# Kernel optimization log

Measured on AMD Instinct MI355X. Metric: run time of the kernel, lower is better.

The kernel has to match this reference:

```python
import jax, jax.numpy as jnp
import numpy as np

H = 16  # heads
DH = 64  # dim_head
SCALE = DH ** -0.5


def rotate_half(x):
    x1, x2 = jnp.split(x, 2, axis=-1)
    return jnp.concatenate([-x2, x1], axis=-1)


def apply_rope(pos, t):
    # pos: [n, d] broadcast over [b, h, n, d]
    return t * jnp.cos(pos) + rotate_half(t) * jnp.sin(pos)


def setup_inputs() -> dict:
    key = jax.random.key(0)
    ks = jax.random.split(key, 6)
    B, N, D = 4, 2048, 1024
    inner = H * DH
    x = jax.random.normal(ks[0], (B, N, D), dtype=jnp.float32)
    rotary_emb = jax.random.normal(ks[1], (N, DH), dtype=jnp.float32)
    Wq = jax.random.normal(ks[2], (D, inner), dtype=jnp.float32) / np.sqrt(D)
    Wkv = jax.random.normal(ks[3], (D, 2 * inner), dtype=jnp.float32) / np.sqrt(D)
    Wout = jax.random.normal(ks[4], (inner, D), dtype=jnp.float32) / np.sqrt(inner)
    bout = jnp.zeros((D,), dtype=jnp.float32)
    return {"x": x, "rotary_emb": rotary_emb, "Wq": Wq, "Wkv": Wkv, "Wout": Wout, "bout": bout}


def reference(x, rotary_emb, Wq, Wkv, Wout, bout):
    B, N, D = x.shape
    # QKV projections (self-attention: context = x)
    q = x @ Wq                       # [b, n, h*d]
    kv = x @ Wkv                     # [b, n, 2*h*d]
    k, v = jnp.split(kv, 2, axis=-1)

    def to_heads(t):
        return t.reshape(B, N, H, DH).transpose(0, 2, 1, 3)  # [b, h, n, d]

    q, k, v = to_heads(q), to_heads(k), to_heads(v)
    q = apply_rope(rotary_emb, q)
    k = apply_rope(rotary_emb, k)

    # scaled dot-product attention
    scores = jnp.einsum('bhid,bhjd->bhij', q, k) * SCALE
    attn = jax.nn.softmax(scores, axis=-1)
    out = jnp.einsum('bhij,bhjd->bhid', attn, v)  # [b, h, n, d]
    out = out.transpose(0, 2, 1, 3).reshape(B, N, H * DH)
    return out @ Wout + bout
```

## Files before the change

kernel.cpp:

```cpp
#include <hip/hip_runtime.h>

#define BB 4
#define NN 2048
#define DD 1024
#define HH 16
#define DHH 64
#define MM (BB*NN)
#define QS 3072

typedef unsigned short u16;
typedef __attribute__((ext_vector_type(8))) short short8;
typedef __attribute__((ext_vector_type(4))) float floatx4;

#if __has_builtin(__builtin_amdgcn_exp2f)
#define EXP2F __builtin_amdgcn_exp2f
#else
#define EXP2F exp2f
#endif

__device__ __forceinline__ u16 f2bf(float f) {
  union { float f; unsigned u; } v; v.f = f;
  unsigned u = v.u;
  return (u16)((u + 0x7fffu + ((u >> 16) & 1u)) >> 16);
}
__device__ __forceinline__ float bf2f(u16 h) {
  union { unsigned u; float f; } v; v.u = ((unsigned)h) << 16;
  return v.f;
}
__device__ __forceinline__ unsigned fbits(float f) {
  union { float f; unsigned u; } v; v.f = f; return v.u;
}
__device__ __forceinline__ unsigned pkbf(float lo, float hi) {
#if __has_builtin(__builtin_amdgcn_perm)
  return __builtin_amdgcn_perm(fbits(hi), fbits(lo), 0x07060302u);
#else
  return (fbits(lo) >> 16) | (fbits(hi) & 0xffff0000u);
#endif
}
__device__ __forceinline__ void gll16(const u16* g, u16* l) {
  __builtin_amdgcn_global_load_lds((const __attribute__((address_space(1))) unsigned int*)g,
                                   (__attribute__((address_space(3))) unsigned int*)l, 16, 0, 0);
}
__device__ __forceinline__ int toff(int row, int kc) {
  int pr = row >> 1;
  int c = (((row & 1) << 2) + kc) ^ (pr & 7);
  return pr * 64 + c * 8;
}

#define SOFTMAX_SCALE 0.18033688f
#define SOFTMAX_BIAS  -28.8539008f

__global__ __launch_bounds__(256) void cvt_kernel(const float* __restrict__ in,
                                                  u16* __restrict__ out, int n) {
  int i = (blockIdx.x * 256 + threadIdx.x) * 4;
  if (i >= n) return;
  float4 v = *(const float4*)(in + i);
  u16 o[4] = {f2bf(v.x), f2bf(v.y), f2bf(v.z), f2bf(v.w)};
  *(uint2*)(out + i) = *(uint2*)o;
}

__global__ __launch_bounds__(256) void tcvt3_kernel(const float* __restrict__ Wq,
                                                    const float* __restrict__ Wkv,
                                                    const float* __restrict__ Wout,
                                                    u16* __restrict__ WT,
                                                    u16* __restrict__ WoutT) {
  __shared__ float t[64][65];
  int bx = blockIdx.x;
  const float* src;
  u16* dst;
  int C, c0;
  if (bx < 16)      { src = Wq;   dst = WT;                       C = 1024; c0 = bx * 64; }
  else if (bx < 48) { src = Wkv;  dst = WT + (size_t)DD * DD;     C = 2048; c0 = (bx - 16) * 64; }
  else              { src = Wout; dst = WoutT;                    C = 1024; c0 = (bx - 48) * 64; }
  const int R = 1024;
  int r0 = blockIdx.y * 64;
  int tid = threadIdx.x;
#pragma unroll
  for (int i = 0; i < 16; ++i) {
    int lin = i * 256 + tid;
    int rr = lin >> 6, cc = lin & 63;
    t[rr][cc] = src[(size_t)(r0 + rr) * C + c0 + cc];
  }
  __syncthreads();
#pragma unroll
  for (int i = 0; i < 16; ++i) {
    int lin = i * 256 + tid;
    int rr = lin >> 6, cc = lin & 63;
    dst[(size_t)(c0 + rr) * R + r0 + cc] = f2bf(t[cc][rr]);
  }
}

__global__ __launch_bounds__(256) void rope_tab_kernel(const float* __restrict__ rot,
                                                       float2* __restrict__ tab) {
  int i = blockIdx.x * 256 + threadIdx.x;
  float p = rot[i];
  float s, c;
  __sincosf(p, &s, &c);
  tab[i] = make_float2(c, s);
}

__global__ __launch_bounds__(512, 2) void gemm_qk(const u16* __restrict__ A,
                                                  const u16* __restrict__ Bt,
                                                  u16* __restrict__ qd,
                                                  u16* __restrict__ kd,
                                                  const float2* __restrict__ tab) {
  const int K = DD;
  const int NT = K / 64;
  __shared__ __align__(16) u16 lds[65536];
  int tid = threadIdx.x;
  int wave = tid >> 6, lane = tid & 63;
  int q4 = lane >> 4, l16 = lane & 15;
  int wr = wave >> 2, wc = wave & 3;

  int flat = blockIdx.y * 8 + blockIdx.x;
  int wg = (flat & 7) * 32 + (flat >> 3);
  int bx = wg & 7, by = wg >> 3;
  int m0 = by * 256, n0 = bx * 256;

  const u16* Ag = A + (size_t)m0 * K;
  const u16* Bg = Bt + (size_t)n0 * K;

  int spr = tid >> 3, sct = tid & 7, su = sct ^ (spr & 7);
  int srow = spr * 2 + (su >> 2);
  int skc = (su & 3) * 8;
  size_t so = (size_t)srow * K + skc;

  int toffA[8], toffB[4];
#pragma unroll
  for (int mi = 0; mi < 8; ++mi) toffA[mi] = wr * 4096 + toff(mi * 16 + l16, q4);
#pragma unroll
  for (int ni = 0; ni < 4; ++ni)
    toffB[ni] = (wc >> 1) * 4096 + toff((wc & 1) * 64 + ni * 16 + l16, q4);

  floatx4 acc[8][4];
#pragma unroll
  for (int mi = 0; mi < 8; ++mi)
#pragma unroll
    for (int ni = 0; ni < 4; ++ni) acc[mi][ni] = (floatx4){0.f, 0.f, 0.f, 0.f};

  auto stageHalf = [&](int t, int mat, int kh) {
    const u16* src = (mat ? Bg : Ag) + so + t * 64 + kh * 32;
    u16* dst = lds + (t & 1) * 32768 + mat * 16384 + kh * 8192 + wave * 512;
    gll16(src, dst);
    gll16(src + (size_t)128 * K, dst + 4096);
  };

  stageHalf(0, 1, 0); stageHalf(0, 0, 0); stageHalf(0, 1, 1); stageHalf(0, 0, 1);
  stageHalf(1, 1, 0); stageHalf(1, 0, 0); stageHalf(1, 1, 1);
  __builtin_amdgcn_s_waitcnt(0x0F76);
  __builtin_amdgcn_s_barrier();

#pragma unroll
  for (int t = 0; t < NT; ++t) {
    const u16* Ab = lds + (t & 1) * 32768;
    const u16* Bb = Ab + 16384;
    short8 af[4], bfq[4];

#pragma unroll
    for (int ni = 0; ni < 4; ++ni) bfq[ni] = *(const short8*)(Bb + toffB[ni]);
#pragma unroll
    for (int f = 0; f < 4; ++f) af[f] = *(const short8*)(Ab + toffA[f]);
    if (t + 1 < NT) stageHalf(t + 1, 0, 1);
    __builtin_amdgcn_s_barrier();
    __builtin_amdgcn_s_waitcnt(0xC07F);
    __builtin_amdgcn_s_setprio(1);
#pragma unroll
    for (int f = 0; f < 4; ++f)
#pragma unroll
      for (int ni = 0; ni < 4; ++ni)
        acc[f][ni] = __builtin_amdgcn_mfma_f32_16x16x32_bf16(bfq[ni], af[f], acc[f][ni], 0, 0, 0);
    __builtin_amdgcn_s_setprio(0);
    __builtin_amdgcn_s_barrier();

#pragma unroll
    for (int f = 0; f < 4; ++f) af[f] = *(const short8*)(Ab + toffA[4 + f]);
    if (t + 2 < NT) stageHalf(t + 2, 1, 0);
    __builtin_amdgcn_s_barrier();
    __builtin_amdgcn_s_waitcnt(0xC07F);
    __builtin_amdgcn_s_setprio(1);
#pragma unroll
    for (int f = 0; f < 4; ++f)
#pragma unroll
      for (int ni = 0; ni < 4; ++ni)
        acc[4 + f][ni] = __builtin_amdgcn_mfma_f32_16x16x32_bf16(bfq[ni], af[f], acc[4 + f][ni], 0, 0, 0);
    __builtin_amdgcn_s_setprio(0);
    __builtin_amdgcn_s_barrier();

#pragma unroll
    for (int ni = 0; ni < 4; ++ni) bfq[ni] = *(const short8*)(Bb + 8192 + toffB[ni]);
#pragma unroll
    for (int f = 0; f < 4; ++f) af[f] = *(const short8*)(Ab + 8192 + toffA[f]);
    if (t + 2 < NT) stageHalf(t + 2, 0, 0);
    __builtin_amdgcn_s_barrier();
    __builtin_amdgcn_s_waitcnt(0xC07F);
    __builtin_amdgcn_s_setprio(1);
#pragma unroll
    for (int f = 0; f < 4; ++f)
#pragma unroll
      for (int ni = 0; ni < 4; ++ni)
        acc[f][ni] = __builtin_amdgcn_mfma_f32_16x16x32_bf16(bfq[ni], af[f], acc[f][ni], 0, 0, 0);
    __builtin_amdgcn_s_setprio(0);
    __builtin_amdgcn_s_barrier();

#pragma unroll
    for (int f = 0; f < 4; ++f) af[f] = *(const short8*)(Ab + 8192 + toffA[4 + f]);
    if (t + 2 < NT) stageHalf(t + 2, 1, 1);
    __builtin_amdgcn_s_barrier();
    __builtin_amdgcn_s_waitcnt(0xC07F);
    __builtin_amdgcn_s_setprio(1);
#pragma unroll
    for (int f = 0; f < 4; ++f)
#pragma unroll
      for (int ni = 0; ni < 4; ++ni)
        acc[4 + f][ni] = __builtin_amdgcn_mfma_f32_16x16x32_bf16(bfq[ni], af[f], acc[4 + f][ni], 0, 0, 0);
    __builtin_amdgcn_s_setprio(0);
    if (t == NT - 2) __builtin_amdgcn_s_waitcnt(0x0F70);
    else if (t < NT - 2) __builtin_amdgcn_s_waitcnt(0x0F76);
    __builtin_amdgcn_s_barrier();
  }

  int h = (n0 + wc * 64) >> 6;
  u16* dst = (h < 16) ? qd : kd;
  int hh = h & 15;
  float scl = (h < 16) ? SOFTMAX_SCALE : 1.0f;
  int b = m0 >> 11;
  int tokbase = (m0 & (NN - 1)) + wr * 128;
#pragma unroll
  for (int mi = 0; mi < 8; ++mi) {
    int tok = tokbase + mi * 16 + l16;
    u16* rowp = dst + ((size_t)(b * HH + hh) * NN + tok) * 64;
    const float2* tb = tab + tok * 64;
#pragma unroll
    for (int ni = 0; ni < 2; ++ni) {
      int d0 = ni * 16 + q4 * 4;
      u16 plo[4], phi[4];
#pragma unroll
      for (int r = 0; r < 4; ++r) {
        float2 cs0 = tb[d0 + r];
        float2 cs1 = tb[d0 + r + 32];
        float v0 = acc[mi][ni][r], v1 = acc[mi][ni + 2][r];
        plo[r] = f2bf((v0 * cs0.x - v1 * cs0.y) * scl);
        phi[r] = f2bf((v1 * cs1.x + v0 * cs1.y) * scl);
      }
      *(uint2*)(rowp + d0) = *(uint2*)plo;
      *(uint2*)(rowp + d0 + 32) = *(uint2*)phi;
    }
  }
}

__global__ __launch_bounds__(256) void gemm_v(const u16* __restrict__ A,
                                              const u16* __restrict__ Bt,
                                              u16* __restrict__ vt) {
  const int K = DD;
  __shared__ __align__(16) u16 lds[16384];
  int tid = threadIdx.x;
  int wave = tid >> 6, lane = tid & 63;
  int q4 = lane >> 4, l16 = lane & 15;

  int flat = blockIdx.y * 8 + blockIdx.x;
  int wg = (flat & 7) * 64 + (flat >> 3);
  int bx = wg & 7, by = wg >> 3;
  int m0 = by * 128, n0 = bx * 128;

  int wm = (wave >> 1) * 64, wn = (wave & 1) * 64;

  const u16* Ag = A + (size_t)m0 * K;
  const u16* Bg = Bt + (size_t)(2048 + n0) * K;
  int o1 = tid, o2 = tid + 256;
  int pr1 = o1 >> 3, c1 = (o1 & 7) ^ (pr1 & 7);
  int row1 = pr1 * 2 + (c1 >> 2), kc1 = (c1 & 3) * 8;
  int pr2 = o2 >> 3, c2 = (o2 & 7) ^ (pr2 & 7);
  int row2 = pr2 * 2 + (c2 >> 2), kc2 = (c2 & 3) * 8;
  int d1 = wave * 512, d2 = 2048 + wave * 512;

  int foA[4], foB[4];
#pragma unroll
  for (int i = 0; i < 4; ++i) {
    foA[i] = toff(wm + i * 16 + l16, q4);
    foB[i] = toff(wn + i * 16 + l16, q4);
  }

  floatx4 acc[4][4];
#pragma unroll
  for (int mi = 0; mi < 4; ++mi)
#pragma unroll
    for (int ni = 0; ni < 4; ++ni) acc[mi][ni] = (floatx4){0.f, 0.f, 0.f, 0.f};

  gll16(Ag + (size_t)row1 * K + kc1, lds + d1);
  gll16(Ag + (size_t)row2 * K + kc2, lds + d2);
  gll16(Bg + (size_t)row1 * K + kc1, lds + 8192 + d1);
  gll16(Bg + (size_t)row2 * K + kc2, lds + 8192 + d2);

  for (int k0 = 0, it = 0; k0 < K; k0 += 32, ++it) {
    int boff = (it & 1) * 4096;
    if (k0 + 32 < K) {
      int nboff = 4096 - boff;
      int kn = k0 + 32;
      gll16(Ag + (size_t)row1 * K + kn + kc1, lds + nboff + d1);
      gll16(Ag + (size_t)row2 * K + kn + kc2, lds + nboff + d2);
      gll16(Bg + (size_t)row1 * K + kn + kc1, lds + 8192 + nboff + d1);
      gll16(Bg + (size_t)row2 * K + kn + kc2, lds + 8192 + nboff + d2);
      __builtin_amdgcn_s_waitcnt(0x0F74);
    } else {
      __builtin_amdgcn_s_waitcnt(0x0F70);
    }
    __builtin_amdgcn_s_barrier();
    const u16* Ac = lds + boff;
    const u16* Bc = lds + 8192 + boff;
    short8 af[4], bfr[4];
#pragma unroll
    for (int i = 0; i < 4; ++i) {
      af[i]  = *(const short8*)(Ac + foA[i]);
      bfr[i] = *(const short8*)(Bc + foB[i]);
    }
#pragma unroll
    for (int mi = 0; mi < 4; ++mi)
#pragma unroll
      for (int ni = 0; ni < 4; ++ni)
        acc[mi][ni] = __builtin_amdgcn_mfma_f32_16x16x32_bf16(af[mi], bfr[ni], acc[mi][ni], 0, 0, 0);
    __builtin_amdgcn_s_barrier();
  }

  int h = (n0 + wn) >> 6;
#pragma unroll
  for (int mi = 0; mi < 4; ++mi) {
    int mbase = m0 + wm + mi * 16 + q4 * 4;
    int b = mbase >> 11;
    int nn = mbase & (NN - 1);
    u16* base = vt + (size_t)(b * HH + h) * (NN * 64) + (nn >> 6) * 4096 + (nn & 63);
#pragma unroll
    for (int ni = 0; ni < 4; ++ni) {
      int d = ni * 16 + l16;
      u16 p[4] = {f2bf(acc[mi][ni][0]), f2bf(acc[mi][ni][1]),
                  f2bf(acc[mi][ni][2]), f2bf(acc[mi][ni][3])};
      *(uint2*)(base + d * 64) = *(uint2*)p;
    }
  }
}

__global__ __launch_bounds__(256) void gemm_out(const u16* __restrict__ A,
                                                const u16* __restrict__ Bt,
                                                float* __restrict__ Cout,
                                                const float* __restrict__ bias,
                                                int M, int N, int K) {
  __shared__ __align__(16) u16 lds[16384];
  int tid = threadIdx.x;
  int wave = tid >> 6, lane = tid & 63;
  int q4 = lane >> 4, l16 = lane & 15;
  int m0 = blockIdx.y * 128, n0 = blockIdx.x * 128;
  int wm = (wave >> 1) * 64, wn = (wave & 1) * 64;

  const u16* Ag = A + (size_t)m0 * K;
  const u16* Bg = Bt + (size_t)n0 * K;
  int o1 = tid, o2 = tid + 256;
  int pr1 = o1 >> 3, c1 = (o1 & 7) ^ (pr1 & 7);
  int row1 = pr1 * 2 + (c1 >> 2), kc1 = (c1 & 3) * 8;
  int pr2 = o2 >> 3, c2 = (o2 & 7) ^ (pr2 & 7);
  int row2 = pr2 * 2 + (c2 >> 2), kc2 = (c2 & 3) * 8;
  int d1 = wave * 512, d2 = 2048 + wave * 512;

  int foA[4], foB[4];
#pragma unroll
  for (int i = 0; i < 4; ++i) {
    foA[i] = toff(wm + i * 16 + l16, q4);
    foB[i] = toff(wn + i * 16 + l16, q4);
  }

  floatx4 acc[4][4];
#pragma unroll
  for (int mi = 0; mi < 4; ++mi)
#pragma unroll
    for (int ni = 0; ni < 4; ++ni) acc[mi][ni] = (floatx4){0.f, 0.f, 0.f, 0.f};

  gll16(Ag + (size_t)row1 * K + kc1, lds + d1);
  gll16(Ag + (size_t)row2 * K + kc2, lds + d2);
  gll16(Bg + (size_t)row1 * K + kc1, lds + 8192 + d1);
  gll16(Bg + (size_t)row2 * K + kc2, lds + 8192 + d2);

  for (int k0 = 0, it = 0; k0 < K; k0 += 32, ++it) {
    int boff = (it & 1) * 4096;
    if (k0 + 32 < K) {
      int nboff = 4096 - boff;
      int kn = k0 + 32;
      gll16(Ag + (size_t)row1 * K + kn + kc1, lds + nboff + d1);
      gll16(Ag + (size_t)row2 * K + kn + kc2, lds + nboff + d2);
      gll16(Bg + (size_t)row1 * K + kn + kc1, lds + 8192 + nboff + d1);
      gll16(Bg + (size_t)row2 * K + kn + kc2, lds + 8192 + nboff + d2);
      __builtin_amdgcn_s_waitcnt(0x0F74);
    } else {
      __builtin_amdgcn_s_waitcnt(0x0F70);
    }
    __builtin_amdgcn_s_barrier();
    const u16* Ac = lds + boff;
    const u16* Bc = lds + 8192 + boff;
    short8 af[4], bfr[4];
#pragma unroll
    for (int i = 0; i < 4; ++i) {
      af[i]  = *(const short8*)(Ac + foA[i]);
      bfr[i] = *(const short8*)(Bc + foB[i]);
    }
#pragma unroll
    for (int mi = 0; mi < 4; ++mi)
#pragma unroll
      for (int ni = 0; ni < 4; ++ni)
        acc[mi][ni] = __builtin_amdgcn_mfma_f32_16x16x32_bf16(af[mi], bfr[ni], acc[mi][ni], 0, 0, 0);
    __builtin_amdgcn_s_barrier();
  }

#pragma unroll
  for (int ni = 0; ni < 4; ++ni) {
    int col = n0 + wn + ni * 16 + l16;
    float bval = bias[col];
#pragma unroll
    for (int mi = 0; mi < 4; ++mi) {
#pragma unroll
      for (int r = 0; r < 4; ++r) {
        int row = m0 + wm + mi * 16 + q4 * 4 + r;
        Cout[(size_t)row * N + col] = acc[mi][ni][r] + bval;
      }
    }
  }
}

__global__ __launch_bounds__(512, 2) void attn_kernel(const u16* __restrict__ qd,
                                                      const u16* __restrict__ kd,
                                                      const u16* __restrict__ vt,
                                                      u16* __restrict__ ao) {
  __shared__ __align__(16) u16 lds[32768];

  int tid = threadIdx.x, wave = tid >> 6, lane = tid & 63;
  int q4 = lane >> 4, l16 = lane & 15;

  int F = blockIdx.y * 4 + blockIdx.x;
  int xcd = F & 7, r = F >> 3;
  int bh = xcd * 8 + (r >> 2);
  int qt = r & 3;
  int b = bh >> 4, h = bh & 15;

  const u16* qbh = qd + (size_t)bh * NN * 64;
  const u16* kbh = kd + (size_t)bh * NN * 64;
  const u16* vbh = vt + (size_t)bh * NN * 64;

  int srow = wave * 8 + (lane >> 3);
  int g = ((lane & 7) ^ ((lane >> 3) & 7)) * 8;
  int prow = ((srow >> 2) & 3) * 8 + ((srow >> 4) & 1) * 4 + (srow & 3) + ((srow >> 5) & 1) * 32;

#pragma unroll
  for (int it = 0; it < 8; ++it)
    gll16(qbh + (size_t)(qt * 512 + it * 64 + srow) * 64 + g, lds + (it * 64 + wave * 8) * 64);
  __builtin_amdgcn_s_waitcnt(0x0F70);
  __builtin_amdgcn_s_barrier();

  short8 aq[4][2];
#pragma unroll
  for (int mi = 0; mi < 4; ++mi)
#pragma unroll
    for (int ks = 0; ks < 2; ++ks) {
      int row = wave * 64 + mi * 16 + l16;
      aq[mi][ks] = *(const short8*)(lds + row * 64 + (((ks * 4 + q4) ^ (row & 7)) * 8));
    }
  __builtin_amdgcn_s_waitcnt(0xC07F);
  __builtin_amdgcn_s_barrier();

  auto stageKV = [&](int t) {
    gll16(kbh + (size_t)(t * 64 + prow) * 64 + g, lds + (t & 3) * 4096 + wave * 512);
    gll16(vbh + (size_t)t * 4096 + srow * 64 + g, lds + 16384 + (t & 3) * 4096 + wave * 512);
  };
  stageKV(0); stageKV(1);

  union { unsigned u[4]; short8 s8; } ones;
#pragma unroll
  for (int i = 0; i < 4; ++i) ones.u[i] = 0x3F803F80u;

  floatx4 lacc[4];
  floatx4 o[4][4];
#pragma unroll
  for (int mi = 0; mi < 4; ++mi) {
    lacc[mi] = (floatx4){0.f, 0.f, 0.f, 0.f};
#pragma unroll
    for (int di = 0; di < 4; ++di) o[mi][di] = (floatx4){0.f, 0.f, 0.f, 0.f};
  }

  const int NT = NN / 64;

  for (int t = 0; t < NT; ++t) {
    if (t < NT - 1) __builtin_amdgcn_s_waitcnt(0x0F72);
    else            __builtin_amdgcn_s_waitcnt(0x0F70);
    __builtin_amdgcn_s_barrier();
    if (t + 2 < NT) stageKV(t + 2);

    const u16* Kc = lds + (t & 3) * 4096;
    const u16* Vc = lds + 16384 + (t & 3) * 4096;

    floatx4 s[4][4];
#pragma unroll
    for (int kg = 0; kg < 4; ++kg)
#pragma unroll
      for (int mi = 0; mi < 4; ++mi)
        s[kg][mi] = (floatx4){SOFTMAX_BIAS, SOFTMAX_BIAS, SOFTMAX_BIAS, SOFTMAX_BIAS};
#pragma unroll
    for (int ks = 0; ks < 2; ++ks) {
      short8 kf[4];
#pragma unroll
      for (int kg = 0; kg < 4; ++kg) {
        int row = kg * 16 + l16;
        kf[kg] = *(const short8*)(Kc + row * 64 + (((ks * 4 + q4) ^ (row & 7)) * 8));
      }
#pragma unroll
      for (int kg = 0; kg < 4; ++kg)
#pragma unroll
        for (int mi = 0; mi < 4; ++mi)
          s[kg][mi] = __builtin_amdgcn_mfma_f32_16x16x32_bf16(kf[kg], aq[mi][ks], s[kg][mi], 0, 0, 0);
    }

    unsigned pk[4][4][2];
#pragma unroll
    for (int kg = 0; kg < 4; ++kg)
#pragma unroll
      for (int mi = 0; mi < 4; ++mi) {
        float e0 = EXP2F(s[kg][mi][0]);
        float e1 = EXP2F(s[kg][mi][1]);
        float e2 = EXP2F(s[kg][mi][2]);
        float e3 = EXP2F(s[kg][mi][3]);
        pk[kg][mi][0] = pkbf(e0, e1);
        pk[kg][mi][1] = pkbf(e2, e3);
      }

#pragma unroll
    for (int ks = 0; ks < 2; ++ks) {
      short8 vf[4];
#pragma unroll
      for (int di = 0; di < 4; ++di) {
        int row = di * 16 + l16;
        vf[di] = *(const short8*)(Vc + row * 64 + (((ks * 4 + q4) ^ (row & 7)) * 8));
      }
#pragma unroll
      for (int mi = 0; mi < 4; ++mi) {
        union { unsigned u[4]; short8 s8; } bw;
        bw.u[0] = pk[2 * ks][mi][0];
        bw.u[1] = pk[2 * ks][mi][1];
        bw.u[2] = pk[2 * ks + 1][mi][0];
        bw.u[3] = pk[2 * ks + 1][mi][1];
        lacc[mi] = __builtin_amdgcn_mfma_f32_16x16x32_bf16(ones.s8, bw.s8, lacc[mi], 0, 0, 0);
#pragma unroll
        for (int di = 0; di < 4; ++di)
          o[mi][di] = __builtin_amdgcn_mfma_f32_16x16x32_bf16(vf[di], bw.s8, o[mi][di], 0, 0, 0);
      }
    }
  }

#pragma unroll
  for (int mi = 0; mi < 4; ++mi) {
    float rinv = 1.0f / lacc[mi][0];
    int qrow = qt * 512 + wave * 64 + mi * 16 + l16;
    size_t base = (size_t)(b * NN + qrow) * DD + h * DHH + q4 * 4;
#pragma unroll
    for (int di = 0; di < 4; ++di) {
      u16 p[4] = {f2bf(o[mi][di][0] * rinv), f2bf(o[mi][di][1] * rinv),
                  f2bf(o[mi][di][2] * rinv), f2bf(o[mi][di][3] * rinv)};
      *(uint2*)(ao + base + di * 16) = *(uint2*)p;
    }
  }
}

extern "C" void kernel_launch(void* const* d_in, const int* in_sizes, int n_in,
                              void* d_out, int out_size, void* d_ws, size_t ws_size,
                              hipStream_t stream) {
  const float* x    = (const float*)d_in[0];
  const float* rot  = (const float*)d_in[1];
  const float* Wq   = (const float*)d_in[2];
  const float* Wkv  = (const float*)d_in[3];
  const float* Wout = (const float*)d_in[4];
  const float* bout = (const float*)d_in[5];
  float* out = (float*)d_out;

  char* ws = (char*)d_ws;
  size_t off = 0;
  auto alloc = [&](size_t bytes) {
    void* p = ws + off;
    off = (off + bytes + 255) & ~(size_t)255;
    return p;
  };
  u16*    xb    = (u16*)alloc((size_t)MM * DD * 2);
  u16*    WT    = (u16*)alloc((size_t)QS * DD * 2);
  u16*    WoutT = (u16*)alloc((size_t)DD * DD * 2);
  float2* tab   = (float2*)alloc((size_t)NN * DHH * 8);
  u16*    qdb   = (u16*)alloc((size_t)MM * DD * 2);
  u16*    kdb   = (u16*)alloc((size_t)MM * DD * 2);
  u16*    vtt   = (u16*)alloc((size_t)MM * DD * 2);
  u16*    ao    = (u16*)alloc((size_t)MM * DD * 2);

  cvt_kernel<<<(MM * DD / 4) / 256, 256, 0, stream>>>(x, xb, MM * DD);
  tcvt3_kernel<<<dim3(64, 16), 256, 0, stream>>>(Wq, Wkv, Wout, WT, WoutT);
  rope_tab_kernel<<<(NN * DHH) / 256, 256, 0, stream>>>(rot, tab);

  gemm_qk<<<dim3(8, 32), 512, 0, stream>>>(xb, WT, qdb, kdb, tab);
  gemm_v<<<dim3(8, 64), 256, 0, stream>>>(xb, WT, vtt);

  attn_kernel<<<dim3(NN / 512, BB * HH), 512, 0, stream>>>(qdb, kdb, vtt, ao);

  gemm_out<<<dim3(DD / 128, MM / 128), 256, 0, stream>>>(ao, WoutT, out, bout, MM, DD, DD);
}
```

Measured before the change: 259.9 us.

## Restructure output GEMM into 256x128 tiles with 8 waves and deeper pipelining

Rewrites the output projection GEMM to use 512-thread blocks computing 256x128 tiles with a K step of 64. It adds a two-stage LDS buffer, interleaves loads of sub-slices with MFMA phases, raises wave priority with setprio, and remaps block IDs across XCDs. Separately, the attention kernel now feeds the softmax bias constant directly as the first MFMA accumulator instead of pre-initialising the score registers. The GEMM change aims to improve data reuse and hide memory latency, at the cost of more LDS (96KB) and more complex barrier and waitcnt logic that must stay correct.

Result: no change. 260.7 us (+0.3%).

```diff
diff --git a/kernel.cpp b/kernel.cpp
--- a/kernel.cpp
+++ b/kernel.cpp
@@ -338,84 +338,138 @@
   }
 }
 
-__global__ __launch_bounds__(256) void gemm_out(const u16* __restrict__ A,
-                                                const u16* __restrict__ Bt,
-                                                float* __restrict__ Cout,
-                                                const float* __restrict__ bias,
-                                                int M, int N, int K) {
-  __shared__ __align__(16) u16 lds[16384];
+__global__ __launch_bounds__(512, 2) void gemm_out(const u16* __restrict__ A,
+                                                   const u16* __restrict__ Bt,
+                                                   float* __restrict__ Cout,
+                                                   const float* __restrict__ bias,
+                                                   int M, int N, int K) {
+  const int NT = DD / 64;
+  __shared__ __align__(16) u16 lds[49152];
   int tid = threadIdx.x;
   int wave = tid >> 6, lane = tid & 63;
   int q4 = lane >> 4, l16 = lane & 15;
-  int m0 = blockIdx.y * 128, n0 = blockIdx.x * 128;
-  int wm = (wave >> 1) * 64, wn = (wave & 1) * 64;
+  int wr = wave >> 2, wc = wave & 3;
+
+  int flat = blockIdx.y * 8 + blockIdx.x;
+  int wg = (flat & 7) * 32 + (flat >> 3);
+  int bx = wg & 7, by = wg >> 3;
+  int m0 = by * 256, n0 = bx * 128;
 
   const u16* Ag = A + (size_t)m0 * K;
   const u16* Bg = Bt + (size_t)n0 * K;
-  int o1 = tid, o2 = tid + 256;
-  int pr1 = o1 >> 3, c1 = (o1 & 7) ^ (pr1 & 7);
-  int row1 = pr1 * 2 + (c1 >> 2), kc1 = (c1 & 3) * 8;
-  int pr2 = o2 >> 3, c2 = (o2 & 7) ^ (pr2 & 7);
-  int row2 = pr2 * 2 + (c2 >> 2), kc2 = (c2 & 3) * 8;
-  int d1 = wave * 512, d2 = 2048 + wave * 512;
-
-  int foA[4], foB[4];
-#pragma unroll
-  for (int i = 0; i < 4; ++i) {
-    foA[i] = toff(wm + i * 16 + l16, q4);
-    foB[i] = toff(wn + i * 16 + l16, q4);
-  }
-
-  floatx4 acc[4][4];
-#pragma unroll
-  for (int mi = 0; mi < 4; ++mi)
-#pragma unroll
-    for (int ni = 0; ni < 4; ++ni) acc[mi][ni] = (floatx4){0.f, 0.f, 0.f, 0.f};
-
-  gll16(Ag + (size_t)row1 * K + kc1, lds + d1);
-  gll16(Ag + (size_t)row2 * K + kc2, lds + d2);
-  gll16(Bg + (size_t)row1 * K + kc1, lds + 8192 + d1);
-  gll16(Bg + (size_t)row2 * K + kc2, lds + 8192 + d2);
-
-  for (int k0 = 0, it = 0; k0 < K; k0 += 32, ++it) {
-    int boff = (it & 1) * 4096;
-    if (k0 + 32 < K) {
-      int nboff = 4096 - boff;
-      int kn = k0 + 32;
-      gll16(Ag + (size_t)row1 * K + kn + kc1, lds + nboff + d1);
-      gll16(Ag + (size_t)row2 * K + kn + kc2, lds + nboff + d2);
-      gll16(Bg + (size_t)row1 * K + kn + kc1, lds + 8192 + nboff + d1);
-      gll16(Bg + (size_t)row2 * K + kn + kc2, lds + 8192 + nboff + d2);
-      __builtin_amdgcn_s_waitcnt(0x0F74);
-    } else {
-      __builtin_amdgcn_s_waitcnt(0x0F70);
-    }
-    __builtin_amdgcn_s_barrier();
-    const u16* Ac = lds + boff;
-    const u16* Bc = lds + 8192 + boff;
-    short8 af[4], bfr[4];
-#pragma unroll
-    for (int i = 0; i < 4; ++i) {
-      af[i]  = *(const short8*)(Ac + foA[i]);
-      bfr[i] = *(const short8*)(Bc + foB[i]);
-    }
-#pragma unroll
-    for (int mi = 0; mi < 4; ++mi)
-#pragma unroll
-      for (int ni = 0; ni < 4; ++ni)
-        acc[mi][ni] = __builtin_amdgcn_mfma_f32_16x16x32_bf16(af[mi], bfr[ni], acc[mi][ni], 0, 0, 0);
-    __builtin_amdgcn_s_barrier();
-  }
-
-#pragma unroll
-  for (int ni = 0; ni < 4; ++ni) {
-    int col = n0 + wn + ni * 16 + l16;
+
+  int spr = tid >> 3, sct = tid & 7, su = sct ^ (spr & 7);
+  int srow = spr * 2 + (su >> 2);
+  int skc = (su & 3) * 8;
+  size_t so = (size_t)srow * K + skc;
+
+  int toffA[8], toffB[2];
+#pragma unroll
+  for (int mi = 0; mi < 8; ++mi) toffA[mi] = wr * 4096 + toff(mi * 16 + l16, q4);
+#pragma unroll
+  for (int ni = 0; ni < 2; ++ni) toffB[ni] = toff(wc * 32 + ni * 16 + l16, q4);
+
+  floatx4 acc[8][2];
+#pragma unroll
+  for (int mi = 0; mi < 8; ++mi)
+#pragma unroll
+    for (int ni = 0; ni < 2; ++ni) acc[mi][ni] = (floatx4){0.f, 0.f, 0.f, 0.f};
+
+  auto stageA = [&](int t, int kh) {
+    const u16* src = Ag + so + t * 64 + kh * 32;
+    u16* dst = lds + (t & 1) * 24576 + kh * 8192 + wave * 512;
+    gll16(src, dst);
+    gll16(src + (size_t)128 * K, dst + 4096);
+  };
+  auto stageB = [&](int t, int kh) {
+    const u16* src = Bg + so + t * 64 + kh * 32;
+    u16* dst = lds + (t & 1) * 24576 + 16384 + kh * 4096 + wave * 512;
+    gll16(src, dst);
+  };
+
+  stageA(0, 0); stageA(0, 1); stageB(0, 0); stageB(0, 1);
+  stageA(1, 0); stageB(1, 0); stageB(1, 1);
+  __builtin_amdgcn_s_waitcnt(0x0F74);
+  __builtin_amdgcn_s_barrier();
+
+#pragma unroll
+  for (int t = 0; t < NT; ++t) {
+    const u16* Ab = lds + (t & 1) * 24576;
+    const u16* Bb = Ab + 16384;
+    short8 af[4], bfq[2];
+
+#pragma unroll
+    for (int ni = 0; ni < 2; ++ni) bfq[ni] = *(const short8*)(Bb + toffB[ni]);
+#pragma unroll
+    for (int f = 0; f < 4; ++f) af[f] = *(const short8*)(Ab + toffA[f]);
+    if (t + 1 < NT) stageA(t + 1, 1);
+    __builtin_amdgcn_s_barrier();
+    __builtin_amdgcn_s_waitcnt(0xC07F);
+    __builtin_amdgcn_s_setprio(1);
+#pragma unroll
+    for (int f = 0; f < 4; ++f)
+#pragma unroll
+      for (int ni = 0; ni < 2; ++ni)
+        acc[f][ni] = __builtin_amdgcn_mfma_f32_16x16x32_bf16(af[f], bfq[ni], acc[f][ni], 0, 0, 0);
+    __builtin_amdgcn_s_setprio(0);
+    __builtin_amdgcn_s_barrier();
+
+#pragma unroll
+    for (int f = 0; f < 4; ++f) af[f] = *(const short8*)(Ab + toffA[4 + f]);
+    if (t + 2 < NT) stageB(t + 2, 0);
+    __builtin_amdgcn_s_barrier();
+    __builtin_amdgcn_s_waitcnt(0xC07F);
+    __builtin_amdgcn_s_setprio(1);
+#pragma unroll
+    for (int f = 0; f < 4; ++f)
+#pragma unroll
+      for (int ni = 0; ni < 2; ++ni)
+        acc[4 + f][ni] = __builtin_amdgcn_mfma_f32_16x16x32_bf16(af[f], bfq[ni], acc[4 + f][ni], 0, 0, 0);
+    __builtin_amdgcn_s_setprio(0);
+    __builtin_amdgcn_s_barrier();
+
+#pragma unroll
+    for (int ni = 0; ni < 2; ++ni) bfq[ni] = *(const short8*)(Bb + 4096 + toffB[ni]);
+#pragma unroll
+    for (int f = 0; f < 4; ++f) af[f] = *(const short8*)(Ab + 8192 + toffA[f]);
+    if (t + 2 < NT) stageA(t + 2, 0);
+    __builtin_amdgcn_s_barrier();
+    __builtin_amdgcn_s_waitcnt(0xC07F);
+    __builtin_amdgcn_s_setprio(1);
+#pragma unroll
+    for (int f = 0; f < 4; ++f)
+#pragma unroll
+      for (int ni = 0; ni < 2; ++ni)
+        acc[f][ni] = __builtin_amdgcn_mfma_f32_16x16x32_bf16(af[f], bfq[ni], acc[f][ni], 0, 0, 0);
+    __builtin_amdgcn_s_setprio(0);
+    __builtin_amdgcn_s_barrier();
+
+#pragma unroll
+    for (int f = 0; f < 4; ++f) af[f] = *(const short8*)(Ab + 8192 + toffA[4 + f]);
+    if (t + 2 < NT) stageB(t + 2, 1);
+    __builtin_amdgcn_s_barrier();
+    __builtin_amdgcn_s_waitcnt(0xC07F);
+    __builtin_amdgcn_s_setprio(1);
+#pragma unroll
+    for (int f = 0; f < 4; ++f)
+#pragma unroll
+      for (int ni = 0; ni < 2; ++ni)
+        acc[4 + f][ni] = __builtin_amdgcn_mfma_f32_16x16x32_bf16(af[f], bfq[ni], acc[4 + f][ni], 0, 0, 0);
+    __builtin_amdgcn_s_setprio(0);
+    if (t == NT - 2) __builtin_amdgcn_s_waitcnt(0x0F70);
+    else if (t < NT - 2) __builtin_amdgcn_s_waitcnt(0x0F74);
+    __builtin_amdgcn_s_barrier();
+  }
+
+#pragma unroll
+  for (int ni = 0; ni < 2; ++ni) {
+    int col = n0 + wc * 32 + ni * 16 + l16;
     float bval = bias[col];
 #pragma unroll
-    for (int mi = 0; mi < 4; ++mi) {
+    for (int mi = 0; mi < 8; ++mi) {
 #pragma unroll
       for (int r = 0; r < 4; ++r) {
-        int row = m0 + wm + mi * 16 + q4 * 4 + r;
+        int row = m0 + wr * 128 + mi * 16 + q4 * 4 + r;
         Cout[(size_t)row * N + col] = acc[mi][ni][r] + bval;
       }
     }
@@ -472,6 +526,8 @@
 #pragma unroll
   for (int i = 0; i < 4; ++i) ones.u[i] = 0x3F803F80u;
 
+  const floatx4 biasc = (floatx4){SOFTMAX_BIAS, SOFTMAX_BIAS, SOFTMAX_BIAS, SOFTMAX_BIAS};
+
   floatx4 lacc[4];
   floatx4 o[4][4];
 #pragma unroll
@@ -493,24 +549,31 @@
     const u16* Vc = lds + 16384 + (t & 3) * 4096;
 
     floatx4 s[4][4];
-#pragma unroll
-    for (int kg = 0; kg < 4; ++kg)
-#pragma unroll
-      for (int mi = 0; mi < 4; ++mi)
-        s[kg][mi] = (floatx4){SOFTMAX_BIAS, SOFTMAX_BIAS, SOFTMAX_BIAS, SOFTMAX_BIAS};
-#pragma unroll
-    for (int ks = 0; ks < 2; ++ks) {
+    {
       short8 kf[4];
 #pragma unroll
       for (int kg = 0; kg < 4; ++kg) {
         int row = kg * 16 + l16;
-        kf[kg] = *(const short8*)(Kc + row * 64 + (((ks * 4 + q4) ^ (row & 7)) * 8));
+        kf[kg] = *(const short8*)(Kc + row * 64 + ((q4 ^ (row & 7)) * 8));
       }
 #pragma unroll
       for (int kg = 0; kg < 4; ++kg)
 #pragma unroll
         for (int mi = 0; mi < 4; ++mi)
-          s[kg][mi] = __builtin_amdgcn_mfma_f32_16x16x32_bf16(kf[kg], aq[mi][ks], s[kg][mi], 0, 0, 0);
+          s[kg][mi] = __builtin_amdgcn_mfma_f32_16x16x32_bf16(kf[kg], aq[mi][0], biasc, 0, 0, 0);
+    }
+    {
+      short8 kf[4];
+#pragma unroll
+      for (int kg = 0; kg < 4; ++kg) {
+        int row = kg * 16 + l16;
+        kf[kg] = *(const short8*)(Kc + row * 64 + (((4 + q4) ^ (row & 7)) * 8));
+      }
+#pragma unroll
+      for (int kg = 0; kg < 4; ++kg)
+#pragma unroll
+        for (int mi = 0; mi < 4; ++mi)
+          s[kg][mi] = __builtin_amdgcn_mfma_f32_16x16x32_bf16(kf[kg], aq[mi][1], s[kg][mi], 0, 0, 0);
     }
 
     unsigned pk[4][4][2];
@@ -599,5 +662,5 @@
 
   attn_kernel<<<dim3(NN / 512, BB * HH), 512, 0, stream>>>(qdb, kdb, vtt, ao);
 
-  gemm_out<<<dim3(DD / 128, MM / 128), 256, 0, stream>>>(ao, WoutT, out, bout, MM, DD, DD);
-}
+  gemm_out<<<dim3(8, 32), 512, 0, stream>>>(ao, WoutT, out, bout, MM, DD, DD);
+}
```
